# Optimization experiments

Hardware: AMD Instinct MI355X
Metric: run time of the kernel (lower is better)

Reference implementation:

```python
import jax, jax.numpy as jnp
import numpy as np
import math

B, L, D = 4, 2048, 1024
NH = 16
HS = D // NH
BLOCK = 2048


def skew(QEr):
    # QEr: [B, nh, L, L] -> relative-position skew trick
    b, nh, nr, nc = QEr.shape
    padded = jnp.pad(QEr, ((0, 0), (0, 0), (0, 0), (1, 0)))  # [B,nh,nr,nc+1]
    reshaped = padded.reshape(b, nh, nc + 1, nr)
    return reshaped[:, :, 1:, :]  # [B,nh,nr,nc]


def setup_inputs() -> dict:
    key = jax.random.key(0)
    ks = jax.random.split(key, 6)
    x = jax.random.normal(ks[0], (B, L, D), dtype=jnp.float32)
    W_attn = jax.random.normal(ks[1], (D, 3 * D), dtype=jnp.float32) * 0.02
    b_attn = jnp.zeros((3 * D,), dtype=jnp.float32)
    Er = jax.random.normal(ks[2], (BLOCK, HS), dtype=jnp.float32)
    W_proj = jax.random.normal(ks[3], (D, D), dtype=jnp.float32) * 0.02
    b_proj = jnp.zeros((D,), dtype=jnp.float32)
    return {"x": x, "W_attn": W_attn, "b_attn": b_attn, "Er": Er,
            "W_proj": W_proj, "b_proj": b_proj}


def reference(x, W_attn, b_attn, Er, W_proj, b_proj):
    b, l, d = x.shape
    qkv = x @ W_attn + b_attn  # [B,L,3D]
    q, k, v = jnp.split(qkv, 3, axis=2)
    # [B,L,D] -> [B,nh,L,hs]
    q = q.reshape(b, l, NH, HS).transpose(0, 2, 1, 3)
    k = k.reshape(b, l, NH, HS).transpose(0, 2, 1, 3)
    v = v.reshape(b, l, NH, HS).transpose(0, 2, 1, 3)

    start = BLOCK - l
    Er_t = Er[start:, :].T  # [hs, L]
    QEr = jnp.einsum('bhld,dm->bhlm', q, Er_t)  # [B,nh,L,L]
    Srel = skew(QEr)

    scale = 1.0 / math.sqrt(HS)
    att = (jnp.einsum('bhld,bhmd->bhlm', q, k) + Srel) * scale
    causal = jnp.tril(jnp.ones((l, l), dtype=bool))
    att = jnp.where(causal[None, None, :, :], att, -jnp.inf)
    att = jax.nn.softmax(att, axis=-1)
    y = jnp.einsum('bhlm,bhmd->bhld', att, v)  # [B,nh,L,hs]
    y = y.transpose(0, 2, 1, 3).reshape(b, l, d)
    return y @ W_proj + b_proj
```

## Files before the change

### kernel.cpp

```cpp
#include <hip/hip_runtime.h>
#include <cstdint>

#define BATCH  4
#define LSEQ   2048
#define DMODEL 1024
#define NHEAD  16
#define HSIZE  64

typedef __attribute__((ext_vector_type(8))) short bf16x8;
typedef __attribute__((ext_vector_type(4))) float f32x4;
typedef unsigned short u16;
typedef unsigned int u32;

__device__ __forceinline__ int xcd_swz(int lin, int n) {
    return (lin & 7) * (n >> 3) + (lin >> 3);
}

__device__ __forceinline__ u16 f2b(float f) {
    unsigned int u = __float_as_uint(f);
    return (u16)((u + 0x7FFFu + ((u >> 16) & 1u)) >> 16);
}
__device__ __forceinline__ float b2f(u16 h) {
    return __uint_as_float(((unsigned int)h) << 16);
}
__device__ __forceinline__ void split2(float x, u16& h, u16& l) {
    h = f2b(x);
    l = f2b(x - b2f(h));
}

__device__ __forceinline__ void gld16(const void* g, void* l) {
    __builtin_amdgcn_global_load_lds(
        (const __attribute__((address_space(1))) unsigned int*)g,
        (__attribute__((address_space(3))) unsigned int*)l, 16, 0, 0);
}

__global__ void split_kernel(const float* __restrict__ in,
                             u16* __restrict__ hi, u16* __restrict__ lo, int n4)
{
    for (int i = blockIdx.x * blockDim.x + threadIdx.x; i < n4;
         i += gridDim.x * blockDim.x) {
        const float4 v = ((const float4*)in)[i];
        ushort4 h, l;
        split2(v.x, h.x, l.x);
        split2(v.y, h.y, l.y);
        split2(v.z, h.z, l.z);
        split2(v.w, h.w, l.w);
        ((ushort4*)hi)[i] = h;
        ((ushort4*)lo)[i] = l;
    }
}

__global__ __launch_bounds__(256)
void splitT_kernel(const float* __restrict__ in,
                   u16* __restrict__ hi, u16* __restrict__ lo, int K, int N)
{
    __shared__ float t[32][33];
    const int k0 = blockIdx.y * 32, n0 = blockIdx.x * 32;
    const int tx = threadIdx.x & 7, ty = threadIdx.x >> 3;

    const float4 v = *(const float4*)(in + (size_t)(k0 + ty) * N + n0 + tx * 4);
    t[ty][tx * 4 + 0] = v.x;
    t[ty][tx * 4 + 1] = v.y;
    t[ty][tx * 4 + 2] = v.z;
    t[ty][tx * 4 + 3] = v.w;
    __syncthreads();

    const float x0 = t[tx * 4 + 0][ty], x1 = t[tx * 4 + 1][ty];
    const float x2 = t[tx * 4 + 2][ty], x3 = t[tx * 4 + 3][ty];
    ushort4 h, l;
    split2(x0, h.x, l.x);
    split2(x1, h.y, l.y);
    split2(x2, h.z, l.z);
    split2(x3, h.w, l.w);
    const size_t o = (size_t)(n0 + ty) * K + k0 + tx * 4;
    *(ushort4*)(hi + o) = h;
    *(ushort4*)(lo + o) = l;
}

template<int MODE>
__global__ __launch_bounds__(256)
void mfma_gemm(const u16* __restrict__ Ah, const u16* __restrict__ Al,
               const u16* __restrict__ Bh, const u16* __restrict__ Bl,
               const float* __restrict__ bias, float* __restrict__ C0,
               u16* __restrict__ Qh, u16* __restrict__ Ql,
               u16* __restrict__ Kh, u16* __restrict__ Kl,
               u16* __restrict__ Vh, u16* __restrict__ Vl,
               int M, int N, int K)
{
    __shared__ __align__(16) u16 sAh[128 * 32];
    __shared__ __align__(16) u16 sAl[128 * 32];
    __shared__ __align__(16) u16 sBh[128 * 32];
    __shared__ __align__(16) u16 sBl[128 * 32];

    const int tid = threadIdx.x;
    const int lane = tid & 63, wave = tid >> 6;
    const int wm = wave >> 1, wn = wave & 1;

    const int gx = gridDim.x;
    int lin = blockIdx.y * gx + blockIdx.x;
    lin = xcd_swz(lin, gx * gridDim.y);
    const int m0 = (lin / gx) * 128, n0 = (lin % gx) * 128;

    f32x4 acc[4][4];
#pragma unroll
    for (int mi = 0; mi < 4; ++mi)
#pragma unroll
        for (int ni = 0; ni < 4; ++ni) {
            acc[mi][ni][0] = 0.f; acc[mi][ni][1] = 0.f;
            acc[mi][ni][2] = 0.f; acc[mi][ni][3] = 0.f;
        }

    const int srow = lane >> 2;
    const int skc8 = (lane & 3) * 8;
    const int r0 = wave * 32;

    for (int kt = 0; kt < K; kt += 32) {
        __syncthreads();
#pragma unroll
        for (int g = 0; g < 2; ++g) {
            const int row = r0 + g * 16 + srow;
            const size_t ga = (size_t)(m0 + row) * K + kt + skc8;
            const size_t gb = (size_t)(n0 + row) * K + kt + skc8;
            u16* la = sAh + (size_t)(r0 + g * 16) * 32;
            u16* lb = sAl + (size_t)(r0 + g * 16) * 32;
            u16* lc = sBh + (size_t)(r0 + g * 16) * 32;
            u16* ld = sBl + (size_t)(r0 + g * 16) * 32;
            gld16(Ah + ga, la);
            gld16(Al + ga, lb);
            gld16(Bh + gb, lc);
            gld16(Bl + gb, ld);
        }
        __syncthreads();

        const int fr = lane & 15, fk8 = (lane >> 4) * 8;
        bf16x8 ah[4], al[4], bh[4], bl[4];
#pragma unroll
        for (int mi = 0; mi < 4; ++mi) {
            const int off = (wm * 64 + mi * 16 + fr) * 32 + fk8;
            ah[mi] = *(const bf16x8*)(sAh + off);
            al[mi] = *(const bf16x8*)(sAl + off);
        }
#pragma unroll
        for (int ni = 0; ni < 4; ++ni) {
            const int off = (wn * 64 + ni * 16 + fr) * 32 + fk8;
            bh[ni] = *(const bf16x8*)(sBh + off);
            bl[ni] = *(const bf16x8*)(sBl + off);
        }
#pragma unroll
        for (int mi = 0; mi < 4; ++mi)
#pragma unroll
            for (int ni = 0; ni < 4; ++ni) {
                acc[mi][ni] = __builtin_amdgcn_mfma_f32_16x16x32_bf16(ah[mi], bh[ni], acc[mi][ni], 0, 0, 0);
                acc[mi][ni] = __builtin_amdgcn_mfma_f32_16x16x32_bf16(ah[mi], bl[ni], acc[mi][ni], 0, 0, 0);
                acc[mi][ni] = __builtin_amdgcn_mfma_f32_16x16x32_bf16(al[mi], bh[ni], acc[mi][ni], 0, 0, 0);
            }
    }

    const int cn = lane & 15, cr = (lane >> 4) * 4;
#pragma unroll
    for (int ni = 0; ni < 4; ++ni) {
        const int col = n0 + wn * 64 + ni * 16 + cn;
        const float bv = bias[col];
        if (MODE == 1) {
#pragma unroll
            for (int mi = 0; mi < 4; ++mi) {
                const int rowb = m0 + wm * 64 + mi * 16 + cr;
#pragma unroll
                for (int r = 0; r < 4; ++r)
                    C0[(size_t)(rowb + r) * N + col] = acc[mi][ni][r] + bv;
            }
        } else {
            const int sel = col >> 10, d = col & 1023;
            const int head = d >> 6, hs = d & 63;
            u16* dh = (sel == 0) ? Qh : (sel == 1) ? Kh : Vh;
            u16* dl = (sel == 0) ? Ql : (sel == 1) ? Kl : Vl;
#pragma unroll
            for (int mi = 0; mi < 4; ++mi) {
                const int rowb = m0 + wm * 64 + mi * 16 + cr;
#pragma unroll
                for (int r = 0; r < 4; ++r) {
                    const int m = rowb + r;
                    const int bb = m >> 11, l = m & (LSEQ - 1);
                    const size_t idx = (((size_t)bb * NHEAD + head) * LSEQ + l) * HSIZE + hs;
                    u16 h, lo;
                    split2(acc[mi][ni][r] + bv, h, lo);
                    dh[idx] = h;
                    dl[idx] = lo;
                }
            }
        }
    }
}

__global__ __launch_bounds__(256)
void attn_kernel(const u16* __restrict__ Qh, const u16* __restrict__ Ql,
                 const u16* __restrict__ Kh, const u16* __restrict__ Kl,
                 const u16* __restrict__ Vh, const u16* __restrict__ Vl,
                 const u16* __restrict__ Eh, const u16* __restrict__ El,
                 u16* __restrict__ Yh, u16* __restrict__ Yl)
{
    const int nqt = LSEQ / 64;
    const int lin = xcd_swz(blockIdx.x, BATCH * NHEAD * nqt);
    const int bh = lin / nqt;
    const int qt = (nqt - 1) - (lin % nqt);
    const int i0 = qt * 64;
    const int bidx = bh >> 4, hidx = bh & 15;

    const size_t bho = (size_t)bh * LSEQ * HSIZE;
    const u16* Qph = Qh + bho; const u16* Qpl = Ql + bho;
    const u16* Kph = Kh + bho; const u16* Kpl = Kl + bho;
    const u16* Vph = Vh + bho; const u16* Vpl = Vl + bho;

    __shared__ __align__(16) unsigned char smem[58624];
    u16* k_h  = (u16*)(smem);
    u16* k_l  = (u16*)(smem + 4096);
    u16* vt_h = (u16*)(smem + 8192);
    u16* vt_l = (u16*)(smem + 12288);
    u16* e_h  = (u16*)(smem + 16384);
    u16* e_l  = (u16*)(smem + 20480);
    u16* p_h  = (u16*)(smem + 24576);
    u16* p_l  = (u16*)(smem + 28672);
    float* ring = (float*)(smem + 32768);

    const int tid = threadIdx.x;
    const int lane = tid & 63, w = tid >> 6;
    const int l4 = lane & 15, lh = lane >> 4;

    bf16x8 aqh[2], aql[2];
#pragma unroll
    for (int ks = 0; ks < 2; ++ks) {
        const size_t qoff = (size_t)(i0 + 16 * w + l4) * 64 + ks * 32 + lh * 8;
        aqh[ks] = *(const bf16x8*)(Qph + qoff);
        aql[ks] = *(const bf16x8*)(Qpl + qoff);
    }

    f32x4 acc_o[4];
#pragma unroll
    for (int i = 0; i < 4; ++i) {
        acc_o[i][0] = 0.f; acc_o[i][1] = 0.f; acc_o[i][2] = 0.f; acc_o[i][3] = 0.f;
    }
    float m_run[4], l_run[4];
#pragma unroll
    for (int i = 0; i < 4; ++i) { m_run[i] = -3.0e38f; l_run[i] = 0.f; }

    const float cexp = 0.18033688011112042f;
    const int e0base = LSEQ - 64 - i0;
    const int ntiles = 2 * qt + 2;

    const int ser = tid >> 3, sec = tid & 7;
    auto stage_er = [&](int g0) {
        const int g = g0 + ser;
        bf16x8 zh = {0, 0, 0, 0, 0, 0, 0, 0}, zl = {0, 0, 0, 0, 0, 0, 0, 0};
        if (g < LSEQ) {
            zh = *(const bf16x8*)(Eh + (size_t)g * 64 + sec * 8);
            zl = *(const bf16x8*)(El + (size_t)g * 64 + sec * 8);
        }
        const int cs = sec ^ (ser & 7);
        *(bf16x8*)(e_h + ser * 64 + cs * 8) = zh;
        *(bf16x8*)(e_l + ser * 64 + cs * 8) = zl;
    };

    auto compute_R = [&](int slotbase) {
        f32x4 racc[2];
#pragma unroll
        for (int i = 0; i < 2; ++i) { racc[i][0]=0.f; racc[i][1]=0.f; racc[i][2]=0.f; racc[i][3]=0.f; }
        __builtin_amdgcn_s_setprio(1);
#pragma unroll
        for (int ks = 0; ks < 2; ++ks)
#pragma unroll
            for (int nf = 0; nf < 2; ++nf) {
                const int re = nf * 16 + l4;
                const int cb = (ks * 4 + lh) ^ (re & 7);
                const bf16x8 beh = *(const bf16x8*)(e_h + re * 64 + cb * 8);
                const bf16x8 bel = *(const bf16x8*)(e_l + re * 64 + cb * 8);
                racc[nf] = __builtin_amdgcn_mfma_f32_16x16x32_bf16(aqh[ks], beh, racc[nf], 0, 0, 0);
                racc[nf] = __builtin_amdgcn_mfma_f32_16x16x32_bf16(aqh[ks], bel, racc[nf], 0, 0, 0);
                racc[nf] = __builtin_amdgcn_mfma_f32_16x16x32_bf16(aql[ks], beh, racc[nf], 0, 0, 0);
            }
        __builtin_amdgcn_s_setprio(0);
#pragma unroll
        for (int nf = 0; nf < 2; ++nf)
#pragma unroll
            for (int r = 0; r < 4; ++r)
                ring[(16 * w + lh * 4 + r) * 101 + slotbase + nf * 16 + l4] = racc[nf][r];
    };

#pragma unroll
    for (int p = 0; p < 2; ++p) {
        __syncthreads();
        stage_er(e0base + 32 * p);
        __syncthreads();
        compute_R(32 * p);
    }

    for (int jt = 0; jt < ntiles; ++jt) {
        const int j0 = jt * 32;
        const int phR = jt % 3;
        const int phW = (jt + 2) % 3;

        __syncthreads();
        {
            const int cs = sec ^ (ser & 7);
            *(bf16x8*)(k_h + ser * 64 + cs * 8) =
                *(const bf16x8*)(Kph + (size_t)(j0 + ser) * 64 + sec * 8);
            *(bf16x8*)(k_l + ser * 64 + cs * 8) =
                *(const bf16x8*)(Kpl + (size_t)(j0 + ser) * 64 + sec * 8);
            const int jp = tid >> 4, d4 = (tid & 15) * 4;
            const ushort4 hA = *(const ushort4*)(Vph + (size_t)(j0 + 2 * jp) * 64 + d4);
            const ushort4 hB = *(const ushort4*)(Vph + (size_t)(j0 + 2 * jp + 1) * 64 + d4);
            const ushort4 lA = *(const ushort4*)(Vpl + (size_t)(j0 + 2 * jp) * 64 + d4);
            const ushort4 lB = *(const ushort4*)(Vpl + (size_t)(j0 + 2 * jp + 1) * 64 + d4);
            const u16 ha[4] = {hA.x, hA.y, hA.z, hA.w}, hb[4] = {hB.x, hB.y, hB.z, hB.w};
            const u16 la[4] = {lA.x, lA.y, lA.z, lA.w}, lb[4] = {lB.x, lB.y, lB.z, lB.w};
            const int cq = jp >> 2, co = jp & 3;
#pragma unroll
            for (int i = 0; i < 4; ++i) {
                const int d = d4 + i;
                const int fd = (d + (d >> 2)) & 3;
                const int cs2 = cq ^ fd;
                *(u32*)(vt_h + d * 32 + cs2 * 8 + co * 2) = (u32)ha[i] | ((u32)hb[i] << 16);
                *(u32*)(vt_l + d * 32 + cs2 * 8 + co * 2) = (u32)la[i] | ((u32)lb[i] << 16);
            }
            stage_er(e0base + 32 * jt + 64);
        }
        __syncthreads();

        f32x4 sacc[2];
#pragma unroll
        for (int i = 0; i < 2; ++i) { sacc[i][0]=0.f; sacc[i][1]=0.f; sacc[i][2]=0.f; sacc[i][3]=0.f; }
        __builtin_amdgcn_s_setprio(1);
#pragma unroll
        for (int ks = 0; ks < 2; ++ks)
#pragma unroll
            for (int cf = 0; cf < 2; ++cf) {
                const int rk = cf * 16 + l4;
                const int cb = (ks * 4 + lh) ^ (rk & 7);
                const bf16x8 bkh = *(const bf16x8*)(k_h + rk * 64 + cb * 8);
                const bf16x8 bkl = *(const bf16x8*)(k_l + rk * 64 + cb * 8);
                sacc[cf] = __builtin_amdgcn_mfma_f32_16x16x32_bf16(aqh[ks], bkh, sacc[cf], 0, 0, 0);
                sacc[cf] = __builtin_amdgcn_mfma_f32_16x16x32_bf16(aqh[ks], bkl, sacc[cf], 0, 0, 0);
                sacc[cf] = __builtin_amdgcn_mfma_f32_16x16x32_bf16(aql[ks], bkh, sacc[cf], 0, 0, 0);
            }
        __builtin_amdgcn_s_setprio(0);

        compute_R(32 * phW);

        float pvv[2][4];
#pragma unroll
        for (int rr = 0; rr < 4; ++rr) {
            const int sr = 16 * w + lh * 4 + rr;
            const int v0 = 32 * phR + 63 + l4 - sr;
            const int s0i = v0 - (v0 >= 96 ? 96 : 0);
            const int v1 = v0 + 16;
            const int s1i = v1 - (v1 >= 96 ? 96 : 0);
            float s0 = sacc[0][rr] + ring[sr * 101 + s0i];
            float s1 = sacc[1][rr] + ring[sr * 101 + s1i];
            if (jt >= 2 * qt) {
                const int joff = j0 - i0;
                if (joff + l4 > sr)      s0 = -3.0e38f;
                if (joff + l4 + 16 > sr) s1 = -3.0e38f;
            }
            float mt = fmaxf(s0, s1);
            mt = fmaxf(mt, __shfl_xor(mt, 1, 16));
            mt = fmaxf(mt, __shfl_xor(mt, 2, 16));
            mt = fmaxf(mt, __shfl_xor(mt, 4, 16));
            mt = fmaxf(mt, __shfl_xor(mt, 8, 16));
            const float mnew  = fmaxf(m_run[rr], mt);
            const float alpha = __builtin_amdgcn_exp2f((m_run[rr] - mnew) * cexp);
            m_run[rr] = mnew;
            const float p0 = __builtin_amdgcn_exp2f((s0 - mnew) * cexp);
            const float p1 = __builtin_amdgcn_exp2f((s1 - mnew) * cexp);
            pvv[0][rr] = p0; pvv[1][rr] = p1;
            float rs = p0 + p1;
            rs += __shfl_xor(rs, 1, 16);
            rs += __shfl_xor(rs, 2, 16);
            rs += __shfl_xor(rs, 4, 16);
            rs += __shfl_xor(rs, 8, 16);
            l_run[rr] = l_run[rr] * alpha + rs;
#pragma unroll
            for (int cfd = 0; cfd < 4; ++cfd) acc_o[cfd][rr] *= alpha;
        }

#pragma unroll
        for (int cf = 0; cf < 2; ++cf)
#pragma unroll
            for (int rr = 0; rr < 4; ++rr) {
                const int pr = 16 * w + lh * 4 + rr;
                const int jc = l4 + 16 * cf;
                const int fp = (pr + (pr >> 2)) & 3;
                const int cs = (jc >> 3) ^ fp;
                u16 h, lo;
                split2(pvv[cf][rr], h, lo);
                p_h[pr * 32 + cs * 8 + (jc & 7)] = h;
                p_l[pr * 32 + cs * 8 + (jc & 7)] = lo;
            }

        {
            const int ap = 16 * w + l4;
            const int ca = lh ^ ((ap + (ap >> 2)) & 3);
            const bf16x8 aph = *(const bf16x8*)(p_h + ap * 32 + ca * 8);
            const bf16x8 apl = *(const bf16x8*)(p_l + ap * 32 + ca * 8);
            __builtin_amdgcn_s_setprio(1);
#pragma unroll
            for (int cfd = 0; cfd < 4; ++cfd) {
                const int rn = cfd * 16 + l4;
                const int cb = lh ^ ((rn + (rn >> 2)) & 3);
                const bf16x8 bvh = *(const bf16x8*)(vt_h + rn * 32 + cb * 8);
                const bf16x8 bvl = *(const bf16x8*)(vt_l + rn * 32 + cb * 8);
                acc_o[cfd] = __builtin_amdgcn_mfma_f32_16x16x32_bf16(aph, bvh, acc_o[cfd], 0, 0, 0);
                acc_o[cfd] = __builtin_amdgcn_mfma_f32_16x16x32_bf16(aph, bvl, acc_o[cfd], 0, 0, 0);
                acc_o[cfd] = __builtin_amdgcn_mfma_f32_16x16x32_bf16(apl, bvh, acc_o[cfd], 0, 0, 0);
            }
            __builtin_amdgcn_s_setprio(0);
        }
    }

#pragma unroll
    for (int rr = 0; rr < 4; ++rr) {
        const float inv = 1.0f / l_run[rr];
        const int row = 16 * w + lh * 4 + rr;
#pragma unroll
        for (int cfd = 0; cfd < 4; ++cfd) {
            const int d = l4 + 16 * cfd;
            u16 h, lo;
            split2(acc_o[cfd][rr] * inv, h, lo);
            const size_t o = ((size_t)(bidx * LSEQ + i0 + row)) * DMODEL + hidx * HSIZE + d;
            Yh[o] = h;
            Yl[o] = lo;
        }
    }
}

extern "C" void kernel_launch(void* const* d_in, const int* in_sizes, int n_in,
                              void* d_out, int out_size, void* d_ws, size_t ws_size,
                              hipStream_t stream)
{
    (void)in_sizes; (void)n_in; (void)out_size; (void)ws_size;
    const float* x      = (const float*)d_in[0];
    const float* W_attn = (const float*)d_in[1];
    const float* b_attn = (const float*)d_in[2];
    const float* Er     = (const float*)d_in[3];
    const float* W_proj = (const float*)d_in[4];
    const float* b_proj = (const float*)d_in[5];
    float* out = (float*)d_out;

    char* ws = (char*)d_ws;
    size_t off = 0;
    const size_t qkvb = (size_t)BATCH * NHEAD * LSEQ * HSIZE * 2;
    u16* qh = (u16*)(ws + off); off += qkvb;
    u16* ql = (u16*)(ws + off); off += qkvb;
    u16* kh = (u16*)(ws + off); off += qkvb;
    u16* kl = (u16*)(ws + off); off += qkvb;
    u16* vh = (u16*)(ws + off); off += qkvb;
    u16* vl = (u16*)(ws + off); off += qkvb;
    u16* xh = (u16*)(ws + off); off += (size_t)BATCH * LSEQ * DMODEL * 2;
    u16* xl = (u16*)(ws + off); off += (size_t)BATCH * LSEQ * DMODEL * 2;
    u16* wah = (u16*)(ws + off); off += (size_t)3 * DMODEL * DMODEL * 2;
    u16* wal = (u16*)(ws + off); off += (size_t)3 * DMODEL * DMODEL * 2;
    u16* wph = (u16*)(ws + off); off += (size_t)DMODEL * DMODEL * 2;
    u16* wpl = (u16*)(ws + off); off += (size_t)DMODEL * DMODEL * 2;
    u16* erh = (u16*)(ws + off); off += (size_t)LSEQ * HSIZE * 2;
    u16* erl = (u16*)(ws + off); off += (size_t)LSEQ * HSIZE * 2;
    u16* yh = xh;
    u16* yl = xl;

    const int M = BATCH * LSEQ;

    split_kernel<<<2048, 256, 0, stream>>>(x, xh, xl, (BATCH * LSEQ * DMODEL) / 4);
    split_kernel<<<128, 256, 0, stream>>>(Er, erh, erl, (LSEQ * HSIZE) / 4);
    splitT_kernel<<<dim3(3 * DMODEL / 32, DMODEL / 32), 256, 0, stream>>>(
        W_attn, wah, wal, DMODEL, 3 * DMODEL);
    splitT_kernel<<<dim3(DMODEL / 32, DMODEL / 32), 256, 0, stream>>>(
        W_proj, wph, wpl, DMODEL, DMODEL);

    mfma_gemm<0><<<dim3(3 * DMODEL / 128, M / 128), 256, 0, stream>>>(
        xh, xl, wah, wal, b_attn, nullptr, qh, ql, kh, kl, vh, vl, M, 3 * DMODEL, DMODEL);

    attn_kernel<<<BATCH * NHEAD * (LSEQ / 64), 256, 0, stream>>>(
        qh, ql, kh, kl, vh, vl, erh, erl, yh, yl);

    mfma_gemm<1><<<dim3(DMODEL / 128, M / 128), 256, 0, stream>>>(
        yh, yl, wph, wpl, b_proj, out, nullptr, nullptr, nullptr, nullptr, nullptr, nullptr,
        M, DMODEL, DMODEL);
}
```

Before: 752.8 us.

## Register-prefetch next K/V/Er tile and alias P buffers onto Er LDS region

Global loads of the next K, V and Er tiles now go into registers right after the staging barrier, so they overlap with the current tile's QK/softmax/PV compute instead of stalling at the top of each iteration. The P buffers now share LDS space with the Er staging buffers, which shrinks shared memory and may allow more resident blocks per CU. Sharing that space requires an extra barrier before P is written, and holding the prefetched tiles raises register pressure.

After: 716.1 us. 1.05x faster.

```diff
diff --git a/kernel.cpp b/kernel.cpp
--- a/kernel.cpp
+++ b/kernel.cpp
@@ -211,16 +211,16 @@
     const u16* Kph = Kh + bho; const u16* Kpl = Kl + bho;
     const u16* Vph = Vh + bho; const u16* Vpl = Vl + bho;
 
-    __shared__ __align__(16) unsigned char smem[58624];
+    __shared__ __align__(16) unsigned char smem[50432];
     u16* k_h  = (u16*)(smem);
     u16* k_l  = (u16*)(smem + 4096);
     u16* vt_h = (u16*)(smem + 8192);
     u16* vt_l = (u16*)(smem + 12288);
     u16* e_h  = (u16*)(smem + 16384);
     u16* e_l  = (u16*)(smem + 20480);
-    u16* p_h  = (u16*)(smem + 24576);
-    u16* p_l  = (u16*)(smem + 28672);
-    float* ring = (float*)(smem + 32768);
+    u16* p_h  = (u16*)(smem + 16384);
+    u16* p_l  = (u16*)(smem + 20480);
+    float* ring = (float*)(smem + 24576);
 
     const int tid = threadIdx.x;
     const int lane = tid & 63, w = tid >> 6;
@@ -248,6 +248,28 @@
     const int ntiles = 2 * qt + 2;
 
     const int ser = tid >> 3, sec = tid & 7;
+    const int jp = tid >> 4, d4v = (tid & 15) * 4;
+
+    bf16x8 pk_h, pk_l, pe_h, pe_l;
+    ushort4 pvA_h, pvB_h, pvA_l, pvB_l;
+    auto prefetch = [&](int jt) {
+        const int j0 = jt * 32;
+        pk_h = *(const bf16x8*)(Kph + (size_t)(j0 + ser) * 64 + sec * 8);
+        pk_l = *(const bf16x8*)(Kpl + (size_t)(j0 + ser) * 64 + sec * 8);
+        pvA_h = *(const ushort4*)(Vph + (size_t)(j0 + 2 * jp) * 64 + d4v);
+        pvB_h = *(const ushort4*)(Vph + (size_t)(j0 + 2 * jp + 1) * 64 + d4v);
+        pvA_l = *(const ushort4*)(Vpl + (size_t)(j0 + 2 * jp) * 64 + d4v);
+        pvB_l = *(const ushort4*)(Vpl + (size_t)(j0 + 2 * jp + 1) * 64 + d4v);
+        const int g = e0base + 32 * jt + 64 + ser;
+        if (g < LSEQ) {
+            pe_h = *(const bf16x8*)(Eh + (size_t)g * 64 + sec * 8);
+            pe_l = *(const bf16x8*)(El + (size_t)g * 64 + sec * 8);
+        } else {
+            pe_h = (bf16x8){0, 0, 0, 0, 0, 0, 0, 0};
+            pe_l = (bf16x8){0, 0, 0, 0, 0, 0, 0, 0};
+        }
+    };
+
     auto stage_er = [&](int g0) {
         const int g = g0 + ser;
         bf16x8 zh = {0, 0, 0, 0, 0, 0, 0, 0}, zl = {0, 0, 0, 0, 0, 0, 0, 0};
@@ -285,6 +307,8 @@
                 ring[(16 * w + lh * 4 + r) * 101 + slotbase + nf * 16 + l4] = racc[nf][r];
     };
 
+    prefetch(0);
+
 #pragma unroll
     for (int p = 0; p < 2; ++p) {
         __syncthreads();
@@ -301,29 +325,27 @@
         __syncthreads();
         {
             const int cs = sec ^ (ser & 7);
-            *(bf16x8*)(k_h + ser * 64 + cs * 8) =
-                *(const bf16x8*)(Kph + (size_t)(j0 + ser) * 64 + sec * 8);
-            *(bf16x8*)(k_l + ser * 64 + cs * 8) =
-                *(const bf16x8*)(Kpl + (size_t)(j0 + ser) * 64 + sec * 8);
-            const int jp = tid >> 4, d4 = (tid & 15) * 4;
-            const ushort4 hA = *(const ushort4*)(Vph + (size_t)(j0 + 2 * jp) * 64 + d4);
-            const ushort4 hB = *(const ushort4*)(Vph + (size_t)(j0 + 2 * jp + 1) * 64 + d4);
-            const ushort4 lA = *(const ushort4*)(Vpl + (size_t)(j0 + 2 * jp) * 64 + d4);
-            const ushort4 lB = *(const ushort4*)(Vpl + (size_t)(j0 + 2 * jp + 1) * 64 + d4);
-            const u16 ha[4] = {hA.x, hA.y, hA.z, hA.w}, hb[4] = {hB.x, hB.y, hB.z, hB.w};
-            const u16 la[4] = {lA.x, lA.y, lA.z, lA.w}, lb[4] = {lB.x, lB.y, lB.z, lB.w};
+            *(bf16x8*)(k_h + ser * 64 + cs * 8) = pk_h;
+            *(bf16x8*)(k_l + ser * 64 + cs * 8) = pk_l;
+            *(bf16x8*)(e_h + ser * 64 + cs * 8) = pe_h;
+            *(bf16x8*)(e_l + ser * 64 + cs * 8) = pe_l;
+            const u16 ha[4] = {pvA_h.x, pvA_h.y, pvA_h.z, pvA_h.w};
+            const u16 hb[4] = {pvB_h.x, pvB_h.y, pvB_h.z, pvB_h.w};
+            const u16 la[4] = {pvA_l.x, pvA_l.y, pvA_l.z, pvA_l.w};
+            const u16 lb[4] = {pvB_l.x, pvB_l.y, pvB_l.z, pvB_l.w};
             const int cq = jp >> 2, co = jp & 3;
 #pragma unroll
             for (int i = 0; i < 4; ++i) {
-                const int d = d4 + i;
+                const int d = d4v + i;
                 const int fd = (d + (d >> 2)) & 3;
                 const int cs2 = cq ^ fd;
                 *(u32*)(vt_h + d * 32 + cs2 * 8 + co * 2) = (u32)ha[i] | ((u32)hb[i] << 16);
                 *(u32*)(vt_l + d * 32 + cs2 * 8 + co * 2) = (u32)la[i] | ((u32)lb[i] << 16);
             }
-            stage_er(e0base + 32 * jt + 64);
-        }
-        __syncthreads();
+        }
+        __syncthreads();
+
+        if (jt + 1 < ntiles) prefetch(jt + 1);
 
         f32x4 sacc[2];
 #pragma unroll
@@ -380,6 +402,8 @@
 #pragma unroll
             for (int cfd = 0; cfd < 4; ++cfd) acc_o[cfd][rr] *= alpha;
         }
+
+        __syncthreads();
 
 #pragma unroll
         for (int cf = 0; cf < 2; ++cf)
```
